# Optimization experiments

Hardware: AMD Instinct MI355X
Metric: run time of the kernel (lower is better)

Reference implementation:

```python
import jax, jax.numpy as jnp
import numpy as np
import math

B_SZ, T, D_IN, D_OUT, N = 8, 4096, 256, 256, 512
RMIN, RMAX, MAX_PHASE = 0.99, 1.0, 6.283


def setup_inputs() -> dict:
    key = jax.random.key(0)
    ks = jax.random.split(key, 8)
    u_in = jax.random.normal(ks[0], (B_SZ, T, D_IN), dtype=jnp.float32)
    u1 = jax.random.uniform(ks[1], (N,), dtype=jnp.float32)
    u2 = jax.random.uniform(ks[2], (N,), dtype=jnp.float32)
    # LRU parametrization from 'Resurrecting Linear Recurrences'
    nu_log = jnp.log(-0.5 * jnp.log(u1 * (RMAX + RMIN) * (RMAX - RMIN) + RMIN ** 2))
    theta_log = jnp.log(MAX_PHASE * u2)
    lambda_mod = jnp.exp(-jnp.exp(nu_log))
    gamma_log = jnp.log(jnp.sqrt(1.0 - jnp.square(lambda_mod)))
    B_real = jax.random.normal(ks[3], (N, D_IN), dtype=jnp.float32) / math.sqrt(2 * D_IN)
    B_imag = jax.random.normal(ks[4], (N, D_IN), dtype=jnp.float32) / math.sqrt(2 * D_IN)
    C_real = jax.random.normal(ks[5], (D_OUT, N), dtype=jnp.float32) / math.sqrt(N)
    C_imag = jax.random.normal(ks[6], (D_OUT, N), dtype=jnp.float32) / math.sqrt(N)
    D = jax.random.normal(ks[7], (D_OUT, D_IN), dtype=jnp.float32) / math.sqrt(D_IN)
    return {"u_in": u_in, "nu_log": nu_log, "theta_log": theta_log,
            "gamma_log": gamma_log, "B_real": B_real, "B_imag": B_imag,
            "C_real": C_real, "C_imag": C_imag, "D": D}


def _lru_forward(u_in, nu_log, theta_log, gamma_log, B_real, B_imag, C_real, C_imag, D):
    lambda_mod = jnp.exp(-jnp.exp(nu_log))
    theta = jnp.exp(theta_log)
    lam = (lambda_mod * jnp.cos(theta) + 1j * lambda_mod * jnp.sin(theta)).astype(jnp.complex64)  # [N]
    gammas = jnp.exp(gamma_log)
    Bc = (B_real + 1j * B_imag).astype(jnp.complex64)  # [N, D_in]
    Cc = (C_real + 1j * C_imag).astype(jnp.complex64)  # [D_out, N]
    # driving term: gamma * (u_t @ B^T)  -> [b, t, n]
    Bu = gammas.astype(jnp.complex64) * jnp.einsum('bti,ni->btn', u_in.astype(jnp.complex64), Bc)
    # linear recurrence x_t = lam * x_{t-1} + Bu_t, x_0 prior = 0, via associative scan
    a = jnp.broadcast_to(lam, Bu.shape)

    def combine(e1, e2):
        a1, b1 = e1
        a2, b2 = e2
        return a1 * a2, a2 * b1 + b2

    _, x = jax.lax.associative_scan(combine, (a, Bu), axis=1)  # [b, t, n] complex
    y = 2.0 * jnp.real(jnp.einsum('btn,on->bto', x, Cc)) + jnp.einsum('bti,oi->bto', u_in, D)
    return y


def reference(u_in, nu_log, theta_log, gamma_log, B_real, B_imag, C_real, C_imag, D):
    return _lru_forward(u_in, nu_log, theta_log, gamma_log, B_real, B_imag, C_real, C_imag, D)
```

## Files before the change

### kernel.cpp

```cpp
#include <hip/hip_runtime.h>
#include <hip/hip_bf16.h>
#include <math.h>

#define B_SZ    8
#define T_LEN   4096
#define DIN     256
#define DOUT    256
#define NST     512
#define M_ROWS  (B_SZ * T_LEN)
#define N1      (2 * NST)
#define K2      (N1 + DIN)
#define CHL     128
#define NCH     (T_LEN / CHL)

typedef __attribute__((ext_vector_type(8))) short bf16x8;
typedef __attribute__((ext_vector_type(4))) float f32x4;
typedef __hip_bfloat16 bf16;

#define OFF_UBF  67108864
#define OFF_WP   83886080
#define OFF_W2   84410368
#define OFF_LAM  85065728
#define OFF_LAML 85069824
#define OFF_SSUM 85073920
#define OFF_PCAR 86122496

__device__ __forceinline__ void gl_lds16(const bf16* g, bf16* l) {
    __builtin_amdgcn_global_load_lds(
        (const __attribute__((address_space(1))) void*)g,
        (__attribute__((address_space(3))) void*)l, 16, 0, 0);
}

__global__ __launch_bounds__(256) void prep(const float* __restrict__ u,
        const float* __restrict__ nu_log, const float* __restrict__ theta_log,
        const float* __restrict__ gamma_log,
        const float* __restrict__ B_real, const float* __restrict__ B_imag,
        const float* __restrict__ C_real, const float* __restrict__ C_imag,
        const float* __restrict__ Dm,
        bf16* __restrict__ ub, bf16* __restrict__ Wp, bf16* __restrict__ W2,
        float* __restrict__ lam, float* __restrict__ lamL) {
    int bid = blockIdx.x, tid = threadIdx.x;
    if (bid < 8192) {
        int i = bid * 256 + tid;
        float4 v = ((const float4*)u)[i];
        union { bf16 h[4]; uint2 u2; } p;
        p.h[0] = __float2bfloat16(v.x); p.h[1] = __float2bfloat16(v.y);
        p.h[2] = __float2bfloat16(v.z); p.h[3] = __float2bfloat16(v.w);
        ((uint2*)ub)[i] = p.u2;
    } else if (bid < 9216) {
        int c = bid - 8192;
        int n = c & (NST - 1);
        float g = expf(gamma_log[n]);
        const float* src = (c < NST) ? (B_real + (size_t)n * DIN)
                                     : (B_imag + (size_t)n * DIN);
        Wp[(size_t)c * DIN + tid] = __float2bfloat16(g * src[tid]);
        int idx = c * 256 + tid;
        if (idx < NST) {
            float lm = expf(-expf(nu_log[idx]));
            float th = expf(theta_log[idx]);
            float lr = lm * cosf(th), li = lm * sinf(th);
            lam[idx] = lr; lam[NST + idx] = li;
            float ar = lr, ai = li;
#pragma unroll
            for (int q = 0; q < 7; ++q) {
                float nr = ar * ar - ai * ai;
                float ni = 2.f * ar * ai;
                ar = nr; ai = ni;
            }
            lamL[idx] = ar; lamL[NST + idx] = ai;
        }
    } else {
        int idx = (bid - 9216) * 256 + tid;
        if (idx < DOUT * K2) {
            int o = idx / K2, c = idx - o * K2;
            float v;
            if (c < NST)            v =  2.0f * C_real[(size_t)o * NST + c];
            else if (c < 2 * NST)   v = -2.0f * C_imag[(size_t)o * NST + (c - NST)];
            else                    v =  Dm[(size_t)o * DIN + (c - 2 * NST)];
            W2[idx] = __float2bfloat16(v);
        }
    }
}

__global__ __launch_bounds__(256) void gemm1(const bf16* __restrict__ u,
                                             const bf16* __restrict__ Wp,
                                             bf16* __restrict__ Bu) {
    __shared__ bf16 As[128 * 32];
    __shared__ bf16 Bs[128 * 32];
    const int tid = threadIdx.x;
    const int m0 = blockIdx.x * 128, n0 = blockIdx.y * 128;
    const int lane = tid & 63, w = tid >> 6;
    const int wm = (w >> 1) * 64, wn = (w & 1) * 64;
    const int lr16 = lane & 15, kq = (lane >> 4) * 8;
    const int srow = tid >> 2, scol = (tid & 3) * 8;

    f32x4 acc[4][4] = {};
    for (int k0 = 0; k0 < DIN; k0 += 32) {
        gl_lds16(u  + (size_t)(m0 + srow) * DIN + k0 + scol,       &As[tid * 8]);
        gl_lds16(u  + (size_t)(m0 + 64 + srow) * DIN + k0 + scol,  &As[2048 + tid * 8]);
        gl_lds16(Wp + (size_t)(n0 + srow) * DIN + k0 + scol,       &Bs[tid * 8]);
        gl_lds16(Wp + (size_t)(n0 + 64 + srow) * DIN + k0 + scol,  &Bs[2048 + tid * 8]);
        __syncthreads();
        bf16x8 af[4], bfr[4];
#pragma unroll
        for (int i = 0; i < 4; ++i)
            af[i] = *(const bf16x8*)(&As[(wm + i * 16 + lr16) * 32 + kq]);
#pragma unroll
        for (int j = 0; j < 4; ++j)
            bfr[j] = *(const bf16x8*)(&Bs[(wn + j * 16 + lr16) * 32 + kq]);
#pragma unroll
        for (int i = 0; i < 4; ++i)
#pragma unroll
            for (int j = 0; j < 4; ++j)
                acc[i][j] = __builtin_amdgcn_mfma_f32_16x16x32_bf16(af[i], bfr[j], acc[i][j], 0, 0, 0);
        __syncthreads();
    }
    const int crow = (lane >> 4) * 4, ccol = lane & 15;
#pragma unroll
    for (int i = 0; i < 4; ++i)
#pragma unroll
        for (int j = 0; j < 4; ++j)
#pragma unroll
            for (int r = 0; r < 4; ++r) {
                int row = m0 + wm + i * 16 + crow + r;
                int col = n0 + wn + j * 16 + ccol;
                Bu[(size_t)row * N1 + col] = __float2bfloat16(acc[i][j][r]);
            }
}

__global__ __launch_bounds__(512) void scan1(const bf16* __restrict__ Bu,
                                             const float* __restrict__ lam,
                                             float* __restrict__ Ssum) {
    int n = threadIdx.x;
    int c = blockIdx.x;
    int b = blockIdx.y;
    float lr = lam[n], li = lam[NST + n];
    const bf16* base = Bu + ((size_t)b * T_LEN + (size_t)c * CHL) * N1;
    float sr = 0.f, si = 0.f;
    for (int j = 0; j < CHL; ++j) {
        float br = __bfloat162float(base[(size_t)j * N1 + n]);
        float bi = __bfloat162float(base[(size_t)j * N1 + NST + n]);
        float tr = lr * sr - li * si + br;
        float ti = lr * si + li * sr + bi;
        sr = tr; si = ti;
    }
    size_t o = ((size_t)b * NCH + c) * N1 + n;
    Ssum[o] = sr; Ssum[o + NST] = si;
}

__global__ __launch_bounds__(256) void scan2(const float* __restrict__ Ssum,
                                             const float* __restrict__ lamL,
                                             float* __restrict__ Pcar) {
    int idx = blockIdx.x * 256 + threadIdx.x;
    int b = idx >> 9, n = idx & (NST - 1);
    float Lr = lamL[n], Li = lamL[NST + n];
    float pr = 0.f, pi = 0.f;
    for (int c = 0; c < NCH; ++c) {
        size_t o = ((size_t)b * NCH + c) * N1 + n;
        Pcar[o] = pr; Pcar[o + NST] = pi;
        float sr = Ssum[o], si = Ssum[o + NST];
        float tr = Lr * pr - Li * pi + sr;
        float ti = Lr * pi + Li * pr + si;
        pr = tr; pi = ti;
    }
}

__global__ __launch_bounds__(512) void scan3(bf16* __restrict__ Bu,
                                             const float* __restrict__ lam,
                                             const float* __restrict__ Pcar) {
    int n = threadIdx.x, c = blockIdx.x, b = blockIdx.y;
    float lr = lam[n], li = lam[NST + n];
    size_t o = ((size_t)b * NCH + c) * N1 + n;
    float xr = Pcar[o], xi = Pcar[o + NST];
    bf16* base = Bu + ((size_t)b * T_LEN + (size_t)c * CHL) * N1;
    for (int j = 0; j < CHL; ++j) {
        float br = __bfloat162float(base[(size_t)j * N1 + n]);
        float bi = __bfloat162float(base[(size_t)j * N1 + NST + n]);
        float tr = lr * xr - li * xi + br;
        float ti = lr * xi + li * xr + bi;
        xr = tr; xi = ti;
        base[(size_t)j * N1 + n]       = __float2bfloat16(xr);
        base[(size_t)j * N1 + NST + n] = __float2bfloat16(xi);
    }
}

__global__ __launch_bounds__(512) void gemm2(const bf16* __restrict__ X,
                                             const bf16* __restrict__ u,
                                             const bf16* __restrict__ W2,
                                             float* __restrict__ y) {
    __shared__ bf16 As[128 * 32];
    __shared__ bf16 Bs[128 * 32];
    const int tid = threadIdx.x;
    const int m0 = blockIdx.x * 128, n0 = blockIdx.y * 128;
    const int lane = tid & 63, w = tid >> 6;
    const int wm = (w >> 2) * 64, wn = (w & 3) * 32;
    const int lr16 = lane & 15, kq = (lane >> 4) * 8;
    const int srow = tid >> 2, scol = (tid & 3) * 8;

    f32x4 acc[4][2] = {};
    for (int k0 = 0; k0 < K2; k0 += 32) {
        const bf16* Asrc; size_t lda; int kc;
        if (k0 < N1) { Asrc = X; lda = N1;  kc = k0; }
        else         { Asrc = u; lda = DIN; kc = k0 - N1; }
        gl_lds16(Asrc + (size_t)(m0 + srow) * lda + kc + scol, &As[tid * 8]);
        gl_lds16(W2 + (size_t)(n0 + srow) * K2 + k0 + scol,    &Bs[tid * 8]);
        __syncthreads();
        bf16x8 af[4], bfr[2];
#pragma unroll
        for (int i = 0; i < 4; ++i)
            af[i] = *(const bf16x8*)(&As[(wm + i * 16 + lr16) * 32 + kq]);
#pragma unroll
        for (int j = 0; j < 2; ++j)
            bfr[j] = *(const bf16x8*)(&Bs[(wn + j * 16 + lr16) * 32 + kq]);
#pragma unroll
        for (int i = 0; i < 4; ++i)
#pragma unroll
            for (int j = 0; j < 2; ++j)
                acc[i][j] = __builtin_amdgcn_mfma_f32_16x16x32_bf16(af[i], bfr[j], acc[i][j], 0, 0, 0);
        __syncthreads();
    }
    const int crow = (lane >> 4) * 4, ccol = lane & 15;
#pragma unroll
    for (int i = 0; i < 4; ++i)
#pragma unroll
        for (int j = 0; j < 2; ++j)
#pragma unroll
            for (int r = 0; r < 4; ++r)
                y[(size_t)(m0 + wm + i * 16 + crow + r) * DOUT + n0 + wn + j * 16 + ccol] = acc[i][j][r];
}

extern "C" void kernel_launch(void* const* d_in, const int* in_sizes, int n_in,
                              void* d_out, int out_size, void* d_ws, size_t ws_size,
                              hipStream_t stream) {
    const float* u_in      = (const float*)d_in[0];
    const float* nu_log    = (const float*)d_in[1];
    const float* theta_log = (const float*)d_in[2];
    const float* gamma_log = (const float*)d_in[3];
    const float* B_real    = (const float*)d_in[4];
    const float* B_imag    = (const float*)d_in[5];
    const float* C_real    = (const float*)d_in[6];
    const float* C_imag    = (const float*)d_in[7];
    const float* Dm        = (const float*)d_in[8];
    float* y = (float*)d_out;
    char* ws = (char*)d_ws;

    bf16*  Bu   = (bf16*)ws;
    bf16*  u_bf = (bf16*)(ws + OFF_UBF);
    bf16*  Wp   = (bf16*)(ws + OFF_WP);
    bf16*  W2   = (bf16*)(ws + OFF_W2);
    float* lam  = (float*)(ws + OFF_LAM);
    float* lamL = (float*)(ws + OFF_LAML);
    float* Ssum = (float*)(ws + OFF_SSUM);
    float* Pcar = (float*)(ws + OFF_PCAR);

    prep<<<10496, 256, 0, stream>>>(u_in, nu_log, theta_log, gamma_log,
                                    B_real, B_imag, C_real, C_imag, Dm,
                                    u_bf, Wp, W2, lam, lamL);
    gemm1<<<dim3(M_ROWS / 128, N1 / 128), 256, 0, stream>>>(u_bf, Wp, Bu);
    scan1<<<dim3(NCH, B_SZ), 512, 0, stream>>>(Bu, lam, Ssum);
    scan2<<<(B_SZ * NST) / 256, 256, 0, stream>>>(Ssum, lamL, Pcar);
    scan3<<<dim3(NCH, B_SZ), 512, 0, stream>>>(Bu, lam, Pcar);
    gemm2<<<dim3(M_ROWS / 128, DOUT / 128), 512, 0, stream>>>(Bu, u_bf, W2, y);
}
```

Baseline: 203.0 us.

## Stage gemm1 output through LDS for coalesced stores; fuse carry scan into scan3

```diff
diff --git a/kernel.cpp b/kernel.cpp
--- a/kernel.cpp
+++ b/kernel.cpp
@@ -23,7 +23,6 @@
 #define OFF_LAM  85065728
 #define OFF_LAML 85069824
 #define OFF_SSUM 85073920
-#define OFF_PCAR 86122496
 
 __device__ __forceinline__ void gl_lds16(const bf16* g, bf16* l) {
     __builtin_amdgcn_global_load_lds(
@@ -87,6 +86,7 @@
                                              bf16* __restrict__ Bu) {
     __shared__ bf16 As[128 * 32];
     __shared__ bf16 Bs[128 * 32];
+    __shared__ bf16 Cs[128 * 136];
     const int tid = threadIdx.x;
     const int m0 = blockIdx.x * 128, n0 = blockIdx.y * 128;
     const int lane = tid & 63, w = tid >> 6;
@@ -121,11 +121,17 @@
 #pragma unroll
         for (int j = 0; j < 4; ++j)
 #pragma unroll
-            for (int r = 0; r < 4; ++r) {
-                int row = m0 + wm + i * 16 + crow + r;
-                int col = n0 + wn + j * 16 + ccol;
-                Bu[(size_t)row * N1 + col] = __float2bfloat16(acc[i][j][r]);
-            }
+            for (int r = 0; r < 4; ++r)
+                Cs[(wm + i * 16 + crow + r) * 136 + wn + j * 16 + ccol] =
+                    __float2bfloat16(acc[i][j][r]);
+    __syncthreads();
+#pragma unroll
+    for (int p = 0; p < 8; ++p) {
+        int row = p * 16 + (tid >> 4);
+        int colg = (tid & 15) * 8;
+        *(uint4*)(&Bu[(size_t)(m0 + row) * N1 + n0 + colg]) =
+            *(const uint4*)(&Cs[row * 136 + colg]);
+    }
 }
 
 __global__ __launch_bounds__(512) void scan1(const bf16* __restrict__ Bu,
@@ -148,30 +154,22 @@
     Ssum[o] = sr; Ssum[o + NST] = si;
 }
 
-__global__ __launch_bounds__(256) void scan2(const float* __restrict__ Ssum,
+__global__ __launch_bounds__(512) void scan3(bf16* __restrict__ Bu,
+                                             const float* __restrict__ lam,
                                              const float* __restrict__ lamL,
-                                             float* __restrict__ Pcar) {
-    int idx = blockIdx.x * 256 + threadIdx.x;
-    int b = idx >> 9, n = idx & (NST - 1);
+                                             const float* __restrict__ Ssum) {
+    int n = threadIdx.x, c = blockIdx.x, b = blockIdx.y;
+    float lr = lam[n], li = lam[NST + n];
     float Lr = lamL[n], Li = lamL[NST + n];
     float pr = 0.f, pi = 0.f;
-    for (int c = 0; c < NCH; ++c) {
-        size_t o = ((size_t)b * NCH + c) * N1 + n;
-        Pcar[o] = pr; Pcar[o + NST] = pi;
+    for (int cp = 0; cp < c; ++cp) {
+        size_t o = ((size_t)b * NCH + cp) * N1 + n;
         float sr = Ssum[o], si = Ssum[o + NST];
         float tr = Lr * pr - Li * pi + sr;
         float ti = Lr * pi + Li * pr + si;
         pr = tr; pi = ti;
     }
-}
-
-__global__ __launch_bounds__(512) void scan3(bf16* __restrict__ Bu,
-                                             const float* __restrict__ lam,
-                                             const float* __restrict__ Pcar) {
-    int n = threadIdx.x, c = blockIdx.x, b = blockIdx.y;
-    float lr = lam[n], li = lam[NST + n];
-    size_t o = ((size_t)b * NCH + c) * N1 + n;
-    float xr = Pcar[o], xi = Pcar[o + NST];
+    float xr = pr, xi = pi;
     bf16* base = Bu + ((size_t)b * T_LEN + (size_t)c * CHL) * N1;
     for (int j = 0; j < CHL; ++j) {
         float br = __bfloat162float(base[(size_t)j * N1 + n]);
@@ -251,14 +249,12 @@
     float* lam  = (float*)(ws + OFF_LAM);
     float* lamL = (float*)(ws + OFF_LAML);
     float* Ssum = (float*)(ws + OFF_SSUM);
-    float* Pcar = (float*)(ws + OFF_PCAR);
 
     prep<<<10496, 256, 0, stream>>>(u_in, nu_log, theta_log, gamma_log,
                                     B_real, B_imag, C_real, C_imag, Dm,
                                     u_bf, Wp, W2, lam, lamL);
     gemm1<<<dim3(M_ROWS / 128, N1 / 128), 256, 0, stream>>>(u_bf, Wp, Bu);
     scan1<<<dim3(NCH, B_SZ), 512, 0, stream>>>(Bu, lam, Ssum);
-    scan2<<<(B_SZ * NST) / 256, 256, 0, stream>>>(Ssum, lamL, Pcar);
-    scan3<<<dim3(NCH, B_SZ), 512, 0, stream>>>(Bu, lam, Pcar);
+    scan3<<<dim3(NCH, B_SZ), 512, 0, stream>>>(Bu, lam, lamL, Ssum);
     gemm2<<<dim3(M_ROWS / 128, DOUT / 128), 512, 0, stream>>>(Bu, u_bf, W2, y);
 }
```

After: 199.0 us. 1.02x faster.
